# Performance work log

Measured on AMD Instinct MI355X. Metric: run time of the kernel, lower is better.

Reference implementation:

```python
import jax, jax.numpy as jnp
import numpy as np

EMBED_DIM = 384
N_DOCS = 262144
BATCH = 64
TOP_K = 8
EPS = 1e-8


def setup_inputs() -> dict:
    key = jax.random.key(0)
    kq, kd = jax.random.split(key)
    query = jax.random.normal(kq, (BATCH, EMBED_DIM), dtype=jnp.float32)
    doc_embeddings = jax.random.normal(kd, (N_DOCS, EMBED_DIM), dtype=jnp.float32)
    return {"query": query, "doc_embeddings": doc_embeddings, "top_k": TOP_K}


def reference(query, doc_embeddings, top_k):
    # Cosine similarity: L2-normalize both sides.
    qn = query / (jnp.linalg.norm(query, axis=-1, keepdims=True) + EPS)          # [B, d]
    dn = doc_embeddings / (jnp.linalg.norm(doc_embeddings, axis=-1, keepdims=True) + EPS)  # [N, d]
    # Similarity scores between every query and every document.
    scores = jnp.einsum('bd,nd->bn', qn, dn)                                      # [B, N]
    # Top-k retrieval.
    topk_scores, topk_idx = jax.lax.top_k(scores, top_k)                          # [B, k]
    # Gather retrieved document embeddings.
    retrieved = dn[topk_idx]                                                      # [B, k, d]
    # Context fusion: softmax-weighted sum of retrieved docs.
    weights = jax.nn.softmax(topk_scores, axis=-1)                                # [B, k]
    fused = jnp.einsum('bk,bkd->bd', weights, retrieved)                          # [B, d]
    return fused, topk_scores, topk_idx
```

## Files before the change

kernel.cpp:

```cpp
#include <hip/hip_runtime.h>
#include <math.h>


#define EMBED 384
#define NDOCS 262144
#define BATCH 64
#define TOPK 8
#define DBLK 128
#define NBLK (NDOCS / DBLK)
#define EPSN 1e-8f
#define SC_STRIDE 132

typedef __attribute__((ext_vector_type(8))) short bf16x8;
typedef __attribute__((ext_vector_type(4))) float f32x4;

#define INS8(s_, i_) do {                                                     \
    if ((s_) > ts[7] || ((s_) == ts[7] && (i_) < ti[7])) {                    \
        ts[7] = (s_); ti[7] = (i_);                                           \
        _Pragma("unroll")                                                     \
        for (int r_ = 7; r_ > 0; --r_) {                                      \
            bool sw_ = (ts[r_] > ts[r_-1]) ||                                 \
                       (ts[r_] == ts[r_-1] && ti[r_] < ti[r_-1]);             \
            float a_ = ts[r_-1]; int b_ = ti[r_-1];                           \
            ts[r_-1] = sw_ ? ts[r_] : a_;  ti[r_-1] = sw_ ? ti[r_] : b_;      \
            ts[r_]   = sw_ ? a_ : ts[r_];  ti[r_]   = sw_ ? b_ : ti[r_];      \
        }                                                                     \
    }                                                                         \
} while (0)

__device__ __forceinline__ void split8v(f32x4 f0, f32x4 f1, bf16x8& bh, bf16x8& bl) {
    float f[8] = {f0[0], f0[1], f0[2], f0[3], f1[0], f1[1], f1[2], f1[3]};
#pragma unroll
    for (int i = 0; i < 8; ++i) {
        unsigned u = __float_as_uint(f[i]);
        unsigned h = (u + 0x7fffu + ((u >> 16) & 1u)) >> 16;
        float fh = __uint_as_float(h << 16);
        float r = f[i] - fh;
        unsigned v = __float_as_uint(r);
        unsigned lo = (v + 0x7fffu + ((v >> 16) & 1u)) >> 16;
        bh[i] = (short)h;
        bl[i] = (short)lo;
    }
}

__device__ __forceinline__ float dot8v(f32x4 f0, f32x4 f1, float s) {
#pragma unroll
    for (int i = 0; i < 4; ++i) s = fmaf(f0[i], f0[i], s);
#pragma unroll
    for (int i = 0; i < 4; ++i) s = fmaf(f1[i], f1[i], s);
    return s;
}

__device__ __forceinline__ int4 gload16(const void* p) {
    int4 r;
    asm volatile("global_load_dwordx4 %0, %1, off" : "=v"(r) : "v"(p) : "memory");
    return r;
}

__device__ __forceinline__ f32x4 dsread16(unsigned a) {
    f32x4 r;
    asm volatile("ds_read_b128 %0, %1" : "=v"(r) : "v"(a) : "memory");
    return r;
}

__global__ void qprep_kernel(const float* __restrict__ q,
                             unsigned short* __restrict__ qh,
                             unsigned short* __restrict__ ql) {
    const int row = blockIdx.x;
    const int lane = threadIdx.x;
    float v[6];
    float s = 0.f;
#pragma unroll
    for (int i = 0; i < 6; ++i) {
        v[i] = q[row * EMBED + lane + 64 * i];
        s = fmaf(v[i], v[i], s);
    }
#pragma unroll
    for (int off = 32; off > 0; off >>= 1) s += __shfl_xor(s, off);
    float rinv = 1.0f / (sqrtf(s) + EPSN);
#pragma unroll
    for (int i = 0; i < 6; ++i) {
        float f = v[i] * rinv;
        unsigned u = __float_as_uint(f);
        unsigned h = (u + 0x7fffu + ((u >> 16) & 1u)) >> 16;
        float fh = __uint_as_float(h << 16);
        float r = f - fh;
        unsigned vv = __float_as_uint(r);
        unsigned lo = (vv + 0x7fffu + ((vv >> 16) & 1u)) >> 16;
        qh[row * EMBED + lane + 64 * i] = (unsigned short)h;
        ql[row * EMBED + lane + 64 * i] = (unsigned short)lo;
    }
}

__global__ __launch_bounds__(256, 4) void score_topk_kernel(
        const float* __restrict__ docs,
        const unsigned short* __restrict__ qh,
        const unsigned short* __restrict__ ql,
        float* __restrict__ pscore, int* __restrict__ pidx) {
    __shared__ __align__(16) char smem[34816];

    const int tid = threadIdx.x;
    const int l = tid & 63;
    const int wv = tid >> 6;
    const int rowl = l & 15;
    const int ksub = l >> 4;
    const int d0 = blockIdx.x * DBLK;

    f32x4 acc[2][4];
#pragma unroll
    for (int s = 0; s < 2; ++s)
#pragma unroll
        for (int m = 0; m < 4; ++m) acc[s][m] = (f32x4){0.f, 0.f, 0.f, 0.f};
    float sq0 = 0.f, sq1 = 0.f;

    const float* sgsrc = docs + (size_t)(d0 + wv * 32 + (l >> 3)) * EMBED
                              + (((l & 7) ^ (l >> 3)) << 2);
    const unsigned short* qhb = qh + rowl * EMBED + ksub * 8;
    const unsigned short* qlb = ql + rowl * EMBED + ksub * 8;

    const unsigned bufb = (unsigned)(uintptr_t)smem;
    const unsigned off00 = wv * 4096 + rowl * 128 + ((ksub * 32 +  0) ^ ((rowl & 7) << 4));
    const unsigned off01 = wv * 4096 + rowl * 128 + ((ksub * 32 + 16) ^ ((rowl & 7) << 4));
    const unsigned off10 = off00 + 2048;
    const unsigned off11 = off01 + 2048;

    {
        float* db = (float*)smem + wv * 1024;
#pragma unroll
        for (int j = 0; j < 4; ++j)
            __builtin_amdgcn_global_load_lds(sgsrc + j * 3072, db + j * 256, 16, 0, 0);
    }

#define SCORE_ITER(KB, DO_STAGE, VM1, VM2)                                     \
    {                                                                          \
        int4 qr[8];                                                            \
        _Pragma("unroll")                                                      \
        for (int m = 0; m < 4; ++m) {                                          \
            qr[m]     = gload16(qhb + m * (16 * EMBED) + (KB) * 32);           \
            qr[4 + m] = gload16(qlb + m * (16 * EMBED) + (KB) * 32);           \
        }                                                                      \
        if (DO_STAGE) {                                                        \
            float* db = (float*)(smem + (((KB) + 1) & 1) * 16384) + wv * 1024; \
            _Pragma("unroll")                                                  \
            for (int j = 0; j < 4; ++j)                                        \
                __builtin_amdgcn_global_load_lds(                              \
                    sgsrc + j * 3072 + ((KB) + 1) * 32, db + j * 256, 16, 0, 0);\
        }                                                                      \
        asm volatile("s_waitcnt " VM1 ::: "memory");                           \
        unsigned pb = bufb + ((KB) & 1) * 16384;                               \
        f32x4 d00 = dsread16(pb + off00);                                      \
        f32x4 d01 = dsread16(pb + off01);                                      \
        f32x4 d10 = dsread16(pb + off10);                                      \
        f32x4 d11 = dsread16(pb + off11);                                      \
        asm volatile("s_waitcnt " VM2 " lgkmcnt(0)" ::: "memory");             \
        __builtin_amdgcn_sched_barrier(0);                                     \
        sq0 = dot8v(d00, d01, sq0);                                            \
        sq1 = dot8v(d10, d11, sq1);                                            \
        bf16x8 bh0, bl0, bh1, bl1;                                             \
        split8v(d00, d01, bh0, bl0);                                           \
        split8v(d10, d11, bh1, bl1);                                           \
        _Pragma("unroll")                                                      \
        for (int m = 0; m < 4; ++m) {                                          \
            bf16x8 ah = *(bf16x8*)&qr[m];                                      \
            bf16x8 al = *(bf16x8*)&qr[4 + m];                                  \
            acc[0][m] = __builtin_amdgcn_mfma_f32_16x16x32_bf16(ah, bh0, acc[0][m], 0, 0, 0); \
            acc[1][m] = __builtin_amdgcn_mfma_f32_16x16x32_bf16(ah, bh1, acc[1][m], 0, 0, 0); \
            acc[0][m] = __builtin_amdgcn_mfma_f32_16x16x32_bf16(al, bh0, acc[0][m], 0, 0, 0); \
            acc[1][m] = __builtin_amdgcn_mfma_f32_16x16x32_bf16(al, bh1, acc[1][m], 0, 0, 0); \
            acc[0][m] = __builtin_amdgcn_mfma_f32_16x16x32_bf16(ah, bl0, acc[0][m], 0, 0, 0); \
            acc[1][m] = __builtin_amdgcn_mfma_f32_16x16x32_bf16(ah, bl1, acc[1][m], 0, 0, 0); \
        }                                                                      \
    }

#pragma unroll 1
    for (int kb = 0; kb < 11; ++kb) {
        SCORE_ITER(kb, 1, "vmcnt(12)", "vmcnt(4)")
    }
    SCORE_ITER(11, 0, "vmcnt(8)", "vmcnt(0)")
#undef SCORE_ITER

    __syncthreads();

    float* S = (float*)smem;
    {
        float t0 = sq0;
        t0 += __shfl_xor(t0, 16);
        t0 += __shfl_xor(t0, 32);
        float rn0 = 1.0f / (sqrtf(t0) + EPSN);
        float t1 = sq1;
        t1 += __shfl_xor(t1, 16);
        t1 += __shfl_xor(t1, 32);
        float rn1 = 1.0f / (sqrtf(t1) + EPSN);
        const int q0 = ksub * 4;
        const int col0 = wv * 32 + rowl;
        const int col1 = col0 + 16;
#pragma unroll
        for (int m = 0; m < 4; ++m) {
            f32x4 a = acc[0][m];
            S[(m * 16 + q0 + 0) * SC_STRIDE + col0] = a[0] * rn0;
            S[(m * 16 + q0 + 1) * SC_STRIDE + col0] = a[1] * rn0;
            S[(m * 16 + q0 + 2) * SC_STRIDE + col0] = a[2] * rn0;
            S[(m * 16 + q0 + 3) * SC_STRIDE + col0] = a[3] * rn0;
            f32x4 b = acc[1][m];
            S[(m * 16 + q0 + 0) * SC_STRIDE + col1] = b[0] * rn1;
            S[(m * 16 + q0 + 1) * SC_STRIDE + col1] = b[1] * rn1;
            S[(m * 16 + q0 + 2) * SC_STRIDE + col1] = b[2] * rn1;
            S[(m * 16 + q0 + 3) * SC_STRIDE + col1] = b[3] * rn1;
        }
    }
    __syncthreads();

    float ts[8]; int ti[8];
#pragma unroll
    for (int r = 0; r < 8; ++r) { ts[r] = -3.402823466e38f; ti[r] = 0x7fffffff; }
    const int sq_ = tid & 63, half = tid >> 6;
    if (tid < 128) {
        for (int ii = 0; ii < 64; ++ii) {
            int d = half * 64 + ((ii + sq_) & 63);
            float sc = S[sq_ * SC_STRIDE + d];
            INS8(sc, d0 + d);
        }
    }
    __syncthreads();
    if (half == 1 && tid < 128) {
#pragma unroll
        for (int r = 0; r < 8; ++r) {
            S[sq_ * 8 + r] = ts[r];
            S[512 + sq_ * 8 + r] = __int_as_float(ti[r]);
        }
    }
    __syncthreads();
    if (tid < 64) {
#pragma unroll
        for (int r = 0; r < 8; ++r) {
            float s2 = S[sq_ * 8 + r];
            int i2 = __float_as_int(S[512 + sq_ * 8 + r]);
            INS8(s2, i2);
        }
        size_t o = ((size_t)sq_ * NBLK + blockIdx.x) * TOPK;
        *(float4*)&pscore[o]     = make_float4(ts[0], ts[1], ts[2], ts[3]);
        *(float4*)&pscore[o + 4] = make_float4(ts[4], ts[5], ts[6], ts[7]);
        *(int4*)&pidx[o]     = make_int4(ti[0], ti[1], ti[2], ti[3]);
        *(int4*)&pidx[o + 4] = make_int4(ti[4], ti[5], ti[6], ti[7]);
    }
}

__global__ __launch_bounds__(256) void merge_a_kernel(
        const float* __restrict__ pscore, const int* __restrict__ pidx,
        float* __restrict__ cs, int* __restrict__ ci) {
    const int q = blockIdx.x >> 3;
    const int c = blockIdx.x & 7;
    const int tid = threadIdx.x;
    __shared__ float ls[2048];
    __shared__ int   li[2048];
    __shared__ float ls2[512];
    __shared__ int   li2[512];
    __shared__ float ls3[64];
    __shared__ int   li3[64];

    {
        size_t o = ((size_t)q * NBLK + c * 256 + tid) * TOPK;
        float4 s0 = *(const float4*)&pscore[o];
        float4 s1 = *(const float4*)&pscore[o + 4];
        int4 i0 = *(const int4*)&pidx[o];
        int4 i1 = *(const int4*)&pidx[o + 4];
        ls[tid * 8 + 0] = s0.x; ls[tid * 8 + 1] = s0.y;
        ls[tid * 8 + 2] = s0.z; ls[tid * 8 + 3] = s0.w;
        ls[tid * 8 + 4] = s1.x; ls[tid * 8 + 5] = s1.y;
        ls[tid * 8 + 6] = s1.z; ls[tid * 8 + 7] = s1.w;
        li[tid * 8 + 0] = i0.x; li[tid * 8 + 1] = i0.y;
        li[tid * 8 + 2] = i0.z; li[tid * 8 + 3] = i0.w;
        li[tid * 8 + 4] = i1.x; li[tid * 8 + 5] = i1.y;
        li[tid * 8 + 6] = i1.z; li[tid * 8 + 7] = i1.w;
    }
    __syncthreads();

    float ts[8]; int ti[8];
    if (tid < 64) {
#pragma unroll
        for (int r = 0; r < 8; ++r) { ts[r] = -3.402823466e38f; ti[r] = 0x7fffffff; }
        for (int e = 0; e < 32; ++e) {
            int k = tid + e * 64;
            float s = ls[k]; int gi = li[k];
            INS8(s, gi);
        }
#pragma unroll
        for (int r = 0; r < 8; ++r) { ls2[tid * 8 + r] = ts[r]; li2[tid * 8 + r] = ti[r]; }
    }
    __syncthreads();
    if (tid < 8) {
#pragma unroll
        for (int r = 0; r < 8; ++r) { ts[r] = -3.402823466e38f; ti[r] = 0x7fffffff; }
        for (int e = 0; e < 64; ++e) {
            int k = tid + e * 8;
            float s = ls2[k]; int gi = li2[k];
            INS8(s, gi);
        }
#pragma unroll
        for (int r = 0; r < 8; ++r) { ls3[tid * 8 + r] = ts[r]; li3[tid * 8 + r] = ti[r]; }
    }
    __syncthreads();
    if (tid == 0) {
#pragma unroll
        for (int r = 0; r < 8; ++r) { ts[r] = -3.402823466e38f; ti[r] = 0x7fffffff; }
        for (int e = 0; e < 64; ++e) {
            float s = ls3[e]; int gi = li3[e];
            INS8(s, gi);
        }
        size_t o = (size_t)(q * 8 + c) * TOPK;
#pragma unroll
        for (int r = 0; r < 8; ++r) { cs[o + r] = ts[r]; ci[o + r] = ti[r]; }
    }
}

__global__ __launch_bounds__(256) void merge_b_kernel(
        const float* __restrict__ docs, const float* __restrict__ cs,
        const int* __restrict__ ci, float* __restrict__ out) {
    const int q = blockIdx.x;
    const int tid = threadIdx.x;
    __shared__ int   fi[TOPK];
    __shared__ float wr[TOPK];

    if (tid == 0) {
        float ts[8]; int ti[8];
#pragma unroll
        for (int r = 0; r < 8; ++r) { ts[r] = -3.402823466e38f; ti[r] = 0x7fffffff; }
        for (int e = 0; e < 64; ++e) {
            float s = cs[q * 64 + e]; int gi = ci[q * 64 + e];
            INS8(s, gi);
        }
        float m = ts[0];
        float w[8]; float sum = 0.f;
#pragma unroll
        for (int r = 0; r < 8; ++r) { w[r] = expf(ts[r] - m); sum += w[r]; }
        float rs = 1.0f / sum;
#pragma unroll
        for (int r = 0; r < 8; ++r) {
            fi[r] = ti[r];
            wr[r] = w[r] * rs;
            out[BATCH * EMBED + q * TOPK + r] = ts[r];
            out[BATCH * EMBED + BATCH * TOPK + q * TOPK + r] = (float)ti[r];
        }
    }
    __syncthreads();

    int lane = tid & 63, wave = tid >> 6;
    for (int r = wave; r < TOPK; r += 4) {
        const float* dp = docs + (size_t)fi[r] * EMBED;
        float s = 0.f;
#pragma unroll
        for (int i = 0; i < 6; ++i) { float v = dp[lane + 64 * i]; s = fmaf(v, v, s); }
#pragma unroll
        for (int off = 32; off > 0; off >>= 1) s += __shfl_xor(s, off);
        if (lane == 0) wr[r] = wr[r] / (sqrtf(s) + EPSN);
    }
    __syncthreads();

    for (int dim = tid; dim < EMBED; dim += 256) {
        float a = 0.f;
#pragma unroll
        for (int r = 0; r < 8; ++r)
            a += wr[r] * docs[(size_t)fi[r] * EMBED + dim];
        out[q * EMBED + dim] = a;
    }
}

extern "C" void kernel_launch(void* const* d_in, const int* in_sizes, int n_in,
                              void* d_out, int out_size, void* d_ws, size_t ws_size,
                              hipStream_t stream) {
    const float* query = (const float*)d_in[0];
    const float* docs  = (const float*)d_in[1];
    float* out = (float*)d_out;

    char* ws = (char*)d_ws;
    unsigned short* qh = (unsigned short*)ws;
    unsigned short* ql = (unsigned short*)(ws + 49152);
    float* pscore = (float*)(ws + 98304);
    int*   pidx   = (int*)(ws + 98304 + (size_t)NBLK * BATCH * TOPK * 4);
    char*  ws3    = ws + 98304 + 2 * (size_t)NBLK * BATCH * TOPK * 4;
    float* cs     = (float*)ws3;
    int*   ci     = (int*)(ws3 + BATCH * 8 * TOPK * 4);

    qprep_kernel<<<64, 64, 0, stream>>>(query, qh, ql);
    score_topk_kernel<<<NBLK, 256, 0, stream>>>(docs, qh, ql, pscore, pidx);
    merge_a_kernel<<<BATCH * 8, 256, 0, stream>>>(pscore, pidx, cs, ci);
    merge_b_kernel<<<BATCH, 256, 0, stream>>>(docs, cs, ci, out);
}
```

Measured before the change: 277.7 us.

## Double doc tile per block and load docs directly into registers, bypassing LDS staging

Each block now scores 256 documents instead of 128, and each wave handles 64 docs with a 4x4 accumulator tile. Document and query fragments are loaded straight from global memory into registers with a double-buffered prefetch (A/B register sets), replacing the async global-to-LDS staging and swizzled LDS reads. Top-k selection now uses all 256 threads, and the merge kernels are resized for half as many partial results. This cuts block count and partial-result traffic and drops LDS round trips, at the cost of much higher register pressure (launch bounds lowered to 2 blocks per SM) and less coalesced row-wise global loads.

```diff
diff --git a/kernel.cpp b/kernel.cpp
--- a/kernel.cpp
+++ b/kernel.cpp
@@ -6,10 +6,10 @@
 #define NDOCS 262144
 #define BATCH 64
 #define TOPK 8
-#define DBLK 128
+#define DBLK 256
 #define NBLK (NDOCS / DBLK)
 #define EPSN 1e-8f
-#define SC_STRIDE 132
+#define SCW 260
 
 typedef __attribute__((ext_vector_type(8))) short bf16x8;
 typedef __attribute__((ext_vector_type(4))) float f32x4;
@@ -28,6 +28,14 @@
     }                                                                         \
 } while (0)
 
+template<int OFF>
+__device__ __forceinline__ int4 gload16o(const void* p) {
+    int4 r;
+    asm volatile("global_load_dwordx4 %0, %1, off offset:%2"
+                 : "=v"(r) : "v"(p), "i"(OFF) : "memory");
+    return r;
+}
+
 __device__ __forceinline__ void split8v(f32x4 f0, f32x4 f1, bf16x8& bh, bf16x8& bl) {
     float f[8] = {f0[0], f0[1], f0[2], f0[3], f1[0], f1[1], f1[2], f1[3]};
 #pragma unroll
@@ -49,18 +57,6 @@
 #pragma unroll
     for (int i = 0; i < 4; ++i) s = fmaf(f1[i], f1[i], s);
     return s;
-}
-
-__device__ __forceinline__ int4 gload16(const void* p) {
-    int4 r;
-    asm volatile("global_load_dwordx4 %0, %1, off" : "=v"(r) : "v"(p) : "memory");
-    return r;
-}
-
-__device__ __forceinline__ f32x4 dsread16(unsigned a) {
-    f32x4 r;
-    asm volatile("ds_read_b128 %0, %1" : "=v"(r) : "v"(a) : "memory");
-    return r;
 }
 
 __global__ void qprep_kernel(const float* __restrict__ q,
@@ -92,12 +88,12 @@
     }
 }
 
-__global__ __launch_bounds__(256, 4) void score_topk_kernel(
+__global__ __launch_bounds__(256, 2) void score_topk_kernel(
         const float* __restrict__ docs,
         const unsigned short* __restrict__ qh,
         const unsigned short* __restrict__ ql,
         float* __restrict__ pscore, int* __restrict__ pidx) {
-    __shared__ __align__(16) char smem[34816];
+    __shared__ float S[BATCH * SCW];
 
     const int tid = threadIdx.x;
     const int l = tid & 63;
@@ -106,106 +102,94 @@
     const int ksub = l >> 4;
     const int d0 = blockIdx.x * DBLK;
 
-    f32x4 acc[2][4];
-#pragma unroll
-    for (int s = 0; s < 2; ++s)
+    f32x4 acc[4][4];
+#pragma unroll
+    for (int s = 0; s < 4; ++s)
 #pragma unroll
         for (int m = 0; m < 4; ++m) acc[s][m] = (f32x4){0.f, 0.f, 0.f, 0.f};
-    float sq0 = 0.f, sq1 = 0.f;
-
-    const float* sgsrc = docs + (size_t)(d0 + wv * 32 + (l >> 3)) * EMBED
-                              + (((l & 7) ^ (l >> 3)) << 2);
-    const unsigned short* qhb = qh + rowl * EMBED + ksub * 8;
-    const unsigned short* qlb = ql + rowl * EMBED + ksub * 8;
-
-    const unsigned bufb = (unsigned)(uintptr_t)smem;
-    const unsigned off00 = wv * 4096 + rowl * 128 + ((ksub * 32 +  0) ^ ((rowl & 7) << 4));
-    const unsigned off01 = wv * 4096 + rowl * 128 + ((ksub * 32 + 16) ^ ((rowl & 7) << 4));
-    const unsigned off10 = off00 + 2048;
-    const unsigned off11 = off01 + 2048;
-
-    {
-        float* db = (float*)smem + wv * 1024;
-#pragma unroll
-        for (int j = 0; j < 4; ++j)
-            __builtin_amdgcn_global_load_lds(sgsrc + j * 3072, db + j * 256, 16, 0, 0);
-    }
-
-#define SCORE_ITER(KB, DO_STAGE, VM1, VM2)                                     \
+    float sq[4] = {0.f, 0.f, 0.f, 0.f};
+
+    const float* dbase[4];
+#pragma unroll
+    for (int s = 0; s < 4; ++s)
+        dbase[s] = docs + (size_t)(d0 + wv * 64 + s * 16 + rowl) * EMBED + ksub * 8;
+    const unsigned short* qb_[8];
+#pragma unroll
+    for (int m = 0; m < 4; ++m) {
+        qb_[m]     = qh + (m * 16 + rowl) * EMBED + ksub * 8;
+        qb_[4 + m] = ql + (m * 16 + rowl) * EMBED + ksub * 8;
+    }
+
+    int4 qA[8], qB[8], dA[8], dB[8];
+
+#pragma unroll
+    for (int m = 0; m < 8; ++m) qA[m] = gload16o<0>(qb_[m]);
+#pragma unroll
+    for (int s = 0; s < 4; ++s) {
+        dA[2 * s]     = gload16o<0>(dbase[s]);
+        dA[2 * s + 1] = gload16o<16>(dbase[s]);
+    }
+
+#define ITER(KB, QC, DC, QN, DN, PF, VM)                                       \
     {                                                                          \
-        int4 qr[8];                                                            \
+        if (PF) {                                                              \
+            _Pragma("unroll")                                                  \
+            for (int m = 0; m < 8; ++m)                                        \
+                QN[m] = gload16o<((KB) + 1) * 64>(qb_[m]);                     \
+            _Pragma("unroll")                                                  \
+            for (int s = 0; s < 4; ++s) {                                      \
+                DN[2 * s]     = gload16o<((KB) + 1) * 128>(dbase[s]);          \
+                DN[2 * s + 1] = gload16o<((KB) + 1) * 128 + 16>(dbase[s]);     \
+            }                                                                  \
+        }                                                                      \
+        asm volatile("s_waitcnt " VM ::: "memory");                            \
+        __builtin_amdgcn_sched_barrier(0);                                     \
         _Pragma("unroll")                                                      \
-        for (int m = 0; m < 4; ++m) {                                          \
-            qr[m]     = gload16(qhb + m * (16 * EMBED) + (KB) * 32);           \
-            qr[4 + m] = gload16(qlb + m * (16 * EMBED) + (KB) * 32);           \
+        for (int s = 0; s < 4; ++s) {                                          \
+            f32x4 fa = *(f32x4*)&DC[2 * s];                                    \
+            f32x4 fb = *(f32x4*)&DC[2 * s + 1];                                \
+            sq[s] = dot8v(fa, fb, sq[s]);                                      \
+            bf16x8 bh, bl;                                                     \
+            split8v(fa, fb, bh, bl);                                           \
+            _Pragma("unroll")                                                  \
+            for (int m = 0; m < 4; ++m) {                                      \
+                bf16x8 ah = *(bf16x8*)&QC[m];                                  \
+                bf16x8 al = *(bf16x8*)&QC[4 + m];                              \
+                acc[s][m] = __builtin_amdgcn_mfma_f32_16x16x32_bf16(ah, bh, acc[s][m], 0, 0, 0); \
+                acc[s][m] = __builtin_amdgcn_mfma_f32_16x16x32_bf16(al, bh, acc[s][m], 0, 0, 0); \
+                acc[s][m] = __builtin_amdgcn_mfma_f32_16x16x32_bf16(ah, bl, acc[s][m], 0, 0, 0); \
+            }                                                                  \
         }                                                                      \
-        if (DO_STAGE) {                                                        \
-            float* db = (float*)(smem + (((KB) + 1) & 1) * 16384) + wv * 1024; \
-            _Pragma("unroll")                                                  \
-            for (int j = 0; j < 4; ++j)                                        \
-                __builtin_amdgcn_global_load_lds(                              \
-                    sgsrc + j * 3072 + ((KB) + 1) * 32, db + j * 256, 16, 0, 0);\
-        }                                                                      \
-        asm volatile("s_waitcnt " VM1 ::: "memory");                           \
-        unsigned pb = bufb + ((KB) & 1) * 16384;                               \
-        f32x4 d00 = dsread16(pb + off00);                                      \
-        f32x4 d01 = dsread16(pb + off01);                                      \
-        f32x4 d10 = dsread16(pb + off10);                                      \
-        f32x4 d11 = dsread16(pb + off11);                                      \
-        asm volatile("s_waitcnt " VM2 " lgkmcnt(0)" ::: "memory");             \
-        __builtin_amdgcn_sched_barrier(0);                                     \
-        sq0 = dot8v(d00, d01, sq0);                                            \
-        sq1 = dot8v(d10, d11, sq1);                                            \
-        bf16x8 bh0, bl0, bh1, bl1;                                             \
-        split8v(d00, d01, bh0, bl0);                                           \
-        split8v(d10, d11, bh1, bl1);                                           \
-        _Pragma("unroll")                                                      \
-        for (int m = 0; m < 4; ++m) {                                          \
-            bf16x8 ah = *(bf16x8*)&qr[m];                                      \
-            bf16x8 al = *(bf16x8*)&qr[4 + m];                                  \
-            acc[0][m] = __builtin_amdgcn_mfma_f32_16x16x32_bf16(ah, bh0, acc[0][m], 0, 0, 0); \
-            acc[1][m] = __builtin_amdgcn_mfma_f32_16x16x32_bf16(ah, bh1, acc[1][m], 0, 0, 0); \
-            acc[0][m] = __builtin_amdgcn_mfma_f32_16x16x32_bf16(al, bh0, acc[0][m], 0, 0, 0); \
-            acc[1][m] = __builtin_amdgcn_mfma_f32_16x16x32_bf16(al, bh1, acc[1][m], 0, 0, 0); \
-            acc[0][m] = __builtin_amdgcn_mfma_f32_16x16x32_bf16(ah, bl0, acc[0][m], 0, 0, 0); \
-            acc[1][m] = __builtin_amdgcn_mfma_f32_16x16x32_bf16(ah, bl1, acc[1][m], 0, 0, 0); \
-        }                                                                      \
-    }
-
-#pragma unroll 1
-    for (int kb = 0; kb < 11; ++kb) {
-        SCORE_ITER(kb, 1, "vmcnt(12)", "vmcnt(4)")
-    }
-    SCORE_ITER(11, 0, "vmcnt(8)", "vmcnt(0)")
-#undef SCORE_ITER
-
-    __syncthreads();
-
-    float* S = (float*)smem;
-    {
-        float t0 = sq0;
-        t0 += __shfl_xor(t0, 16);
-        t0 += __shfl_xor(t0, 32);
-        float rn0 = 1.0f / (sqrtf(t0) + EPSN);
-        float t1 = sq1;
-        t1 += __shfl_xor(t1, 16);
-        t1 += __shfl_xor(t1, 32);
-        float rn1 = 1.0f / (sqrtf(t1) + EPSN);
+    }
+
+    ITER(0,  qA, dA, qB, dB, 1, "vmcnt(16)")
+    ITER(1,  qB, dB, qA, dA, 1, "vmcnt(16)")
+    ITER(2,  qA, dA, qB, dB, 1, "vmcnt(16)")
+    ITER(3,  qB, dB, qA, dA, 1, "vmcnt(16)")
+    ITER(4,  qA, dA, qB, dB, 1, "vmcnt(16)")
+    ITER(5,  qB, dB, qA, dA, 1, "vmcnt(16)")
+    ITER(6,  qA, dA, qB, dB, 1, "vmcnt(16)")
+    ITER(7,  qB, dB, qA, dA, 1, "vmcnt(16)")
+    ITER(8,  qA, dA, qB, dB, 1, "vmcnt(16)")
+    ITER(9,  qB, dB, qA, dA, 1, "vmcnt(16)")
+    ITER(10, qA, dA, qB, dB, 1, "vmcnt(16)")
+    ITER(11, qB, dB, qA, dA, 0, "vmcnt(0)")
+#undef ITER
+
+#pragma unroll
+    for (int s = 0; s < 4; ++s) {
+        float t = sq[s];
+        t += __shfl_xor(t, 16);
+        t += __shfl_xor(t, 32);
+        float rn = 1.0f / (sqrtf(t) + EPSN);
+        const int col = wv * 64 + s * 16 + rowl;
         const int q0 = ksub * 4;
-        const int col0 = wv * 32 + rowl;
-        const int col1 = col0 + 16;
 #pragma unroll
         for (int m = 0; m < 4; ++m) {
-            f32x4 a = acc[0][m];
-            S[(m * 16 + q0 + 0) * SC_STRIDE + col0] = a[0] * rn0;
-            S[(m * 16 + q0 + 1) * SC_STRIDE + col0] = a[1] * rn0;
-            S[(m * 16 + q0 + 2) * SC_STRIDE + col0] = a[2] * rn0;
-            S[(m * 16 + q0 + 3) * SC_STRIDE + col0] = a[3] * rn0;
-            f32x4 b = acc[1][m];
-            S[(m * 16 + q0 + 0) * SC_STRIDE + col1] = b[0] * rn1;
-            S[(m * 16 + q0 + 1) * SC_STRIDE + col1] = b[1] * rn1;
-            S[(m * 16 + q0 + 2) * SC_STRIDE + col1] = b[2] * rn1;
-            S[(m * 16 + q0 + 3) * SC_STRIDE + col1] = b[3] * rn1;
+            f32x4 a = acc[s][m];
+#pragma unroll
+            for (int j = 0; j < 4; ++j)
+                S[(m * 16 + q0 + j) * SCW + col] = a[j] * rn;
         }
     }
     __syncthreads();
@@ -213,31 +197,31 @@
     float ts[8]; int ti[8];
 #pragma unroll
     for (int r = 0; r < 8; ++r) { ts[r] = -3.402823466e38f; ti[r] = 0x7fffffff; }
-    const int sq_ = tid & 63, half = tid >> 6;
-    if (tid < 128) {
-        for (int ii = 0; ii < 64; ++ii) {
-            int d = half * 64 + ((ii + sq_) & 63);
-            float sc = S[sq_ * SC_STRIDE + d];
-            INS8(sc, d0 + d);
-        }
-    }
-    __syncthreads();
-    if (half == 1 && tid < 128) {
-#pragma unroll
-        for (int r = 0; r < 8; ++r) {
-            S[sq_ * 8 + r] = ts[r];
-            S[512 + sq_ * 8 + r] = __int_as_float(ti[r]);
-        }
+    const int q = tid & 63, qa = tid >> 6;
+    for (int ii = 0; ii < 64; ++ii) {
+        int d = qa * 64 + ((ii + q) & 63);
+        float sc = S[q * SCW + d];
+        INS8(sc, d0 + d);
+    }
+    __syncthreads();
+#pragma unroll
+    for (int r = 0; r < 8; ++r) {
+        S[(qa * 64 + q) * 8 + r] = ts[r];
+        S[2048 + (qa * 64 + q) * 8 + r] = __int_as_float(ti[r]);
     }
     __syncthreads();
     if (tid < 64) {
 #pragma unroll
-        for (int r = 0; r < 8; ++r) {
-            float s2 = S[sq_ * 8 + r];
-            int i2 = __float_as_int(S[512 + sq_ * 8 + r]);
-            INS8(s2, i2);
-        }
-        size_t o = ((size_t)sq_ * NBLK + blockIdx.x) * TOPK;
+        for (int r = 0; r < 8; ++r) { ts[r] = -3.402823466e38f; ti[r] = 0x7fffffff; }
+        for (int a = 0; a < 4; ++a) {
+#pragma unroll
+            for (int r = 0; r < 8; ++r) {
+                float s2 = S[(a * 64 + q) * 8 + r];
+                int i2 = __float_as_int(S[2048 + (a * 64 + q) * 8 + r]);
+                INS8(s2, i2);
+            }
+        }
+        size_t o = ((size_t)q * NBLK + blockIdx.x) * TOPK;
         *(float4*)&pscore[o]     = make_float4(ts[0], ts[1], ts[2], ts[3]);
         *(float4*)&pscore[o + 4] = make_float4(ts[4], ts[5], ts[6], ts[7]);
         *(int4*)&pidx[o]     = make_int4(ti[0], ti[1], ti[2], ti[3]);
@@ -248,8 +232,8 @@
 __global__ __launch_bounds__(256) void merge_a_kernel(
         const float* __restrict__ pscore, const int* __restrict__ pidx,
         float* __restrict__ cs, int* __restrict__ ci) {
-    const int q = blockIdx.x >> 3;
-    const int c = blockIdx.x & 7;
+    const int q = blockIdx.x >> 2;
+    const int c = blockIdx.x & 3;
     const int tid = threadIdx.x;
     __shared__ float ls[2048];
     __shared__ int   li[2048];
@@ -307,7 +291,7 @@
             float s = ls3[e]; int gi = li3[e];
             INS8(s, gi);
         }
-        size_t o = (size_t)(q * 8 + c) * TOPK;
+        size_t o = (size_t)(q * 4 + c) * TOPK;
 #pragma unroll
         for (int r = 0; r < 8; ++r) { cs[o + r] = ts[r]; ci[o + r] = ti[r]; }
     }
@@ -325,8 +309,8 @@
         float ts[8]; int ti[8];
 #pragma unroll
         for (int r = 0; r < 8; ++r) { ts[r] = -3.402823466e38f; ti[r] = 0x7fffffff; }
-        for (int e = 0; e < 64; ++e) {
-            float s = cs[q * 64 + e]; int gi = ci[q * 64 + e];
+        for (int e = 0; e < 32; ++e) {
+            float s = cs[q * 32 + e]; int gi = ci[q * 32 + e];
             INS8(s, gi);
         }
         float m = ts[0];
@@ -379,10 +363,10 @@
     int*   pidx   = (int*)(ws + 98304 + (size_t)NBLK * BATCH * TOPK * 4);
     char*  ws3    = ws + 98304 + 2 * (size_t)NBLK * BATCH * TOPK * 4;
     float* cs     = (float*)ws3;
-    int*   ci     = (int*)(ws3 + BATCH * 8 * TOPK * 4);
+    int*   ci     = (int*)(ws3 + BATCH * 4 * TOPK * 4);
 
     qprep_kernel<<<64, 64, 0, stream>>>(query, qh, ql);
     score_topk_kernel<<<NBLK, 256, 0, stream>>>(docs, qh, ql, pscore, pidx);
-    merge_a_kernel<<<BATCH * 8, 256, 0, stream>>>(pscore, pidx, cs, ci);
+    merge_a_kernel<<<BATCH * 4, 256, 0, stream>>>(pscore, pidx, cs, ci);
     merge_b_kernel<<<BATCH, 256, 0, stream>>>(docs, cs, ci, out);
 }
```

After: 238.9 us. 14.0% less time.
